# Performance work log

Hardware: AMD Instinct MI355X
Metric: run time of the kernel (lower is better)

## Reference

```python
import jax, jax.numpy as jnp
import numpy as np
import math

DROPOUT_P = 0.1

def setup_inputs() -> dict:
    key = jax.random.key(0)
    k1, k2, k3 = jax.random.split(key, 3)
    B, Lq, Lk, D = 8, 2048, 2048, 128
    x1 = jax.random.normal(k1, (B, Lq, D), dtype=jnp.float32)
    x2 = jax.random.normal(k2, (B, Lk, D), dtype=jnp.float32)
    qm = jnp.zeros((1, Lq, Lk), dtype=jnp.float32)  # additive attention mask
    u = jax.random.uniform(k3, (B, Lq, Lk), dtype=jnp.float32)  # dropout uniforms
    return {"x1": x1, "x2": x2, "qm": qm, "u": u}

def reference(x1, x2, qm, u):
    # scaled dot-product attention with additive mask + inverted dropout
    scale = 1.0 / math.sqrt(x1.shape[-1])
    qk = jnp.einsum('bqd,bkd->bqk', x1, x2) * scale + qm  # [B, Lq, Lk]
    attn = jax.nn.softmax(qk, axis=-1)
    keep = (u >= DROPOUT_P).astype(attn.dtype) / (1.0 - DROPOUT_P)
    attn = attn * keep
    out = jnp.einsum('bqk,bkd->bqd', attn, x2)  # [B, Lq, D]
    return out
```

## Files before the change

kernel.cpp:

```cpp
#include <hip/hip_runtime.h>
#include <hip/hip_bf16.h>
#include <stdint.h>

#define LQ 2048
#define LK 2048
#define DH 128
#define BQ 64
#define KB 128
#define NT (LK / KB)
#define KROW 136
#define LOG2E 1.44269504088896340736f
#define QSCALE 0.088388347648318447f

typedef __attribute__((ext_vector_type(8)))  short bf16x8;
typedef __attribute__((ext_vector_type(16))) float f32x16;
typedef __attribute__((ext_vector_type(4)))  float f32x4;

union FragAB { uint32_t u[4]; bf16x8 v; };

__device__ __forceinline__ uint32_t pack2_bf16(float lo, float hi) {
  union { __hip_bfloat16 b; uint16_t u; } a, c;
  a.b = __float2bfloat16(lo);
  c.b = __float2bfloat16(hi);
  return (uint32_t)a.u | ((uint32_t)c.u << 16);
}

__global__ __launch_bounds__(256)
void mask_kernel(const float* __restrict__ uu, uint32_t* __restrict__ maskp) {
  const int lane = threadIdx.x & 63;
  const int wid  = blockIdx.x * 4 + (threadIdx.x >> 6);
#pragma unroll 1
  for (int i = 0; i < 16; ++i) {
    const size_t F = ((size_t)i * 8192 + wid) * 256;
    float u0 = uu[F + 0 * 64 + lane];
    float u1 = uu[F + 1 * 64 + lane];
    float u2 = uu[F + 2 * 64 + lane];
    float u3 = uu[F + 3 * 64 + lane];
    uint64_t B0 = __ballot(u0 >= 0.1f);
    uint64_t B1 = __ballot(u1 >= 0.1f);
    uint64_t B2 = __ballot(u2 >= 0.1f);
    uint64_t B3 = __ballot(u3 >= 0.1f);
    if (lane < 8) {
      const int m = lane;
      uint64_t bb = (m < 2) ? B0 : (m < 4) ? B1 : (m < 6) ? B2 : B3;
      uint32_t val = (m & 1) ? (uint32_t)(bb >> 32) : (uint32_t)bb;
      const size_t row = F >> 11;
      const int c = (int)((F >> 5) & 63) + m;
      maskp[row * 64 + (size_t)((c & 3) * 16 + (c >> 2))] = val;
    }
  }
}

__global__ __launch_bounds__(256)
void qmt_kernel(const float* __restrict__ qm, uint16_t* __restrict__ qmt2) {
  const int kc = threadIdx.x & 63;
  const int q  = blockIdx.x * 4 + (threadIdx.x >> 6);
  f32x4 r[8];
  const float* src = qm + (size_t)q * 2048 + kc * 32;
#pragma unroll
  for (int c = 0; c < 8; ++c) r[c] = *(const f32x4*)(src + c * 4);
#pragma unroll
  for (int h = 0; h < 2; ++h) {
    uint32_t w[8];
#pragma unroll
    for (int i = 0; i < 8; ++i) {
      const int gi0 = 2 * i, gi1 = 2 * i + 1;
      const float v0 = r[h + (gi0 >> 2) * 2][gi0 & 3] * LOG2E;
      const float v1 = r[h + (gi1 >> 2) * 2][gi1 & 3] * LOG2E;
      w[i] = pack2_bf16(v0, v1);
    }
    uint16_t* dst = qmt2 + ((size_t)(kc * 2 + h) * 2048 + q) * 16;
    uint4 lo = {w[0], w[1], w[2], w[3]};
    uint4 hi = {w[4], w[5], w[6], w[7]};
    *(uint4*)dst = lo;
    *(uint4*)(dst + 8) = hi;
  }
}

__device__ __forceinline__ void stage_writes(uint16_t* Kb, uint16_t* Vb,
                                             const f32x4* st, int sbi, int sbj) {
#pragma unroll
  for (int j = 0; j < 2; ++j) {
    const int rowb = 4 * (sbi + 16 * j);
#pragma unroll
    for (int r = 0; r < 4; ++r) {
      f32x4 v = st[j * 4 + r];
      uint64_t pk = (uint64_t)pack2_bf16(v.x, v.y) |
                    ((uint64_t)pack2_bf16(v.z, v.w) << 32);
      *(uint64_t*)(Kb + (size_t)(rowb + r) * KROW + 4 * sbj) = pk;
    }
#pragma unroll
    for (int c = 0; c < 4; ++c) {
      uint64_t pv = (uint64_t)pack2_bf16(st[j * 4 + 0][c], st[j * 4 + 1][c]) |
                    ((uint64_t)pack2_bf16(st[j * 4 + 2][c], st[j * 4 + 3][c]) << 32);
      *(uint64_t*)(Vb + (size_t)(4 * sbj + c) * KROW + rowb) = pv;
    }
  }
}

__global__ __launch_bounds__(512, 2)
void fattn_kernel(const float* __restrict__ x1, const float* __restrict__ x2,
                  const uint32_t* __restrict__ maskp,
                  const uint16_t* __restrict__ qmt2,
                  float* __restrict__ out)
{
  __shared__ uint16_t ldsK[2][128 * KROW];
  __shared__ uint16_t ldsV[2][128 * KROW];

  const int tid  = threadIdx.x;
  const int wv   = tid >> 6;
  const int lane = tid & 63;
  const int ln   = lane & 31;
  const int h    = lane >> 5;
  const int qsub = wv & 1;
  const int ks   = wv >> 1;

  const int b    = blockIdx.x & 7;
  const int qblk = blockIdx.x >> 3;
  const int qrow = qblk * BQ + qsub * 32 + ln;

  FragAB qf[8];
  {
    const float* qp = x1 + ((size_t)(b * LQ + qrow)) * DH + h * 8;
    const float qs = QSCALE * LOG2E;
#pragma unroll
    for (int dc = 0; dc < 8; ++dc) {
      f32x4 a = *(const f32x4*)(qp + dc * 16);
      f32x4 c = *(const f32x4*)(qp + dc * 16 + 4);
      qf[dc].u[0] = pack2_bf16(a.x * qs, a.y * qs);
      qf[dc].u[1] = pack2_bf16(a.z * qs, a.w * qs);
      qf[dc].u[2] = pack2_bf16(c.x * qs, c.y * qs);
      qf[dc].u[3] = pack2_bf16(c.z * qs, c.w * qs);
    }
  }

  const int sbi = tid >> 5;
  const int sbj = tid & 31;
  const float* x2base = x2 + (size_t)b * LK * DH + sbj * 4;
  const uint32_t* maskrow = maskp + ((size_t)(b * LQ + qrow)) * 64 + ks * 16;

  f32x4 st[8];
#pragma unroll
  for (int j = 0; j < 2; ++j)
#pragma unroll
    for (int r = 0; r < 4; ++r)
      st[j * 4 + r] = *(const f32x4*)(x2base + (size_t)(4 * (sbi + 16 * j) + r) * DH);

  uint32_t mcur = maskrow[0];
  uint4 qc0, qc1;
  {
    const uint16_t* qp16 = qmt2 + (((size_t)(0 * 4 + ks) * 2 + h) * 2048 + qrow) * 16;
    qc0 = *(const uint4*)qp16;
    qc1 = *(const uint4*)(qp16 + 8);
  }

  stage_writes(ldsK[0], ldsV[0], st, sbi, sbj);
  __syncthreads();

  float m_run = -1e30f, l_run = 0.f;
  f32x16 acco[4];
#pragma unroll
  for (int d2 = 0; d2 < 4; ++d2)
#pragma unroll
    for (int i = 0; i < 16; ++i) acco[d2][i] = 0.f;

  for (int t = 0; t < NT; ++t) {
    const int cb = t & 1;
    const uint16_t* Kb = ldsK[cb];
    const uint16_t* Vb = ldsV[cb];
    const int kb = t * KB;

    uint32_t mnxt = 0; uint4 qn0, qn1;
    if (t + 1 < NT) {
#pragma unroll
      for (int j = 0; j < 2; ++j)
#pragma unroll
        for (int r = 0; r < 4; ++r)
          st[j * 4 + r] = *(const f32x4*)(x2base + (size_t)(kb + KB + 4 * (sbi + 16 * j) + r) * DH);
      mnxt = maskrow[t + 1];
      const uint16_t* qp16 = qmt2 + (((size_t)((t + 1) * 4 + ks) * 2 + h) * 2048 + qrow) * 16;
      qn0 = *(const uint4*)qp16;
      qn1 = *(const uint4*)(qp16 + 8);
    }

    f32x16 sacc;
#pragma unroll
    for (int i = 0; i < 16; ++i) sacc[i] = 0.f;
    const uint16_t* Krow = Kb + (size_t)(ks * 32 + ln) * KROW + h * 8;
#pragma unroll
    for (int dc = 0; dc < 8; ++dc) {
      bf16x8 af = *(const bf16x8*)(Krow + dc * 16);
      sacc = __builtin_amdgcn_mfma_f32_32x32x16_bf16(af, qf[dc].v, sacc, 0, 0, 0);
    }

#define ADDQM(W, I) { sacc[I] += __uint_as_float((W) << 16); \
                      sacc[I + 1] += __uint_as_float((W) & 0xffff0000u); }
    ADDQM(qc0.x, 0)  ADDQM(qc0.y, 2)  ADDQM(qc0.z, 4)  ADDQM(qc0.w, 6)
    ADDQM(qc1.x, 8)  ADDQM(qc1.y, 10) ADDQM(qc1.z, 12) ADDQM(qc1.w, 14)
#undef ADDQM

    float pm = sacc[0];
#pragma unroll
    for (int i = 1; i < 16; ++i) pm = fmaxf(pm, sacc[i]);
    pm = fmaxf(pm, __shfl_xor(pm, 32));
    const float mnew = fmaxf(m_run, pm);
    const float resc = __builtin_amdgcn_exp2f(m_run - mnew);
    m_run = mnew;
    float rs = 0.f;
#pragma unroll
    for (int i = 0; i < 16; ++i) {
      sacc[i] = __builtin_amdgcn_exp2f(sacc[i] - mnew);
      rs += sacc[i];
    }
    rs += __shfl_xor(rs, 32);
    l_run = l_run * resc + rs;

#pragma unroll
    for (int g = 0; g < 4; ++g)
#pragma unroll
      for (int j2 = 0; j2 < 4; ++j2) {
        const uint32_t keep = (mcur >> (h * 4 + g * 8 + j2)) & 1u;
        sacc[g * 4 + j2] = keep ? sacc[g * 4 + j2] : 0.f;
      }

    uint32_t pr[4][2], sw[4][2];
#pragma unroll
    for (int g = 0; g < 4; ++g) {
      pr[g][0] = pack2_bf16(sacc[4 * g + 0], sacc[4 * g + 1]);
      pr[g][1] = pack2_bf16(sacc[4 * g + 2], sacc[4 * g + 3]);
      sw[g][0] = __shfl_xor(pr[g][0], 32);
      sw[g][1] = __shfl_xor(pr[g][1], 32);
    }
    FragAB bfr[2];
#pragma unroll
    for (int c = 0; c < 2; ++c) {
      bfr[c].u[0] = h ? sw[2 * c + 1][0] : pr[2 * c][0];
      bfr[c].u[1] = h ? sw[2 * c + 1][1] : pr[2 * c][1];
      bfr[c].u[2] = h ? pr[2 * c + 1][0] : sw[2 * c][0];
      bfr[c].u[3] = h ? pr[2 * c + 1][1] : sw[2 * c][1];
    }

#pragma unroll
    for (int d2 = 0; d2 < 4; ++d2)
#pragma unroll
      for (int i = 0; i < 16; ++i) acco[d2][i] *= resc;

#pragma unroll
    for (int d2 = 0; d2 < 4; ++d2) {
      const uint16_t* Vrow = Vb + (size_t)(d2 * 32 + ln) * KROW + ks * 32 + h * 8;
#pragma unroll
      for (int c = 0; c < 2; ++c) {
        bf16x8 av = *(const bf16x8*)(Vrow + c * 16);
        acco[d2] = __builtin_amdgcn_mfma_f32_32x32x16_bf16(av, bfr[c].v, acco[d2], 0, 0, 0);
      }
    }

    if (t + 1 < NT) {
      stage_writes(ldsK[cb ^ 1], ldsV[cb ^ 1], st, sbi, sbj);
      mcur = mnxt; qc0 = qn0; qc1 = qn1;
    }
    __syncthreads();
  }

  float* scr = (wv < 4) ? ((float*)ldsK + (size_t)wv * 4224)
                        : ((float*)ldsV + (size_t)(wv - 4) * 4224);
  scr[lane]      = m_run;
  scr[64 + lane] = l_run;
#pragma unroll
  for (int d2 = 0; d2 < 4; ++d2)
#pragma unroll
    for (int g = 0; g < 4; ++g) {
      f32x4 vv;
#pragma unroll
      for (int j2 = 0; j2 < 4; ++j2) vv[j2] = acco[d2][g * 4 + j2];
      *(f32x4*)(scr + 128 + (size_t)(d2 * 4 + g) * 256 + lane * 4) = vv;
    }
  __syncthreads();

  if (wv < 2) {
    const float* rg[4];
#pragma unroll
    for (int s2 = 0; s2 < 4; ++s2) {
      const int r = qsub + 2 * s2;
      rg[s2] = (r < 4) ? ((const float*)ldsK + (size_t)r * 4224)
                       : ((const float*)ldsV + (size_t)(r - 4) * 4224);
    }
    const float ms0 = rg[0][lane], ms1 = rg[1][lane], ms2 = rg[2][lane], ms3 = rg[3][lane];
    const float ls0 = rg[0][64 + lane], ls1 = rg[1][64 + lane];
    const float ls2 = rg[2][64 + lane], ls3 = rg[3][64 + lane];
    const float mM = fmaxf(fmaxf(ms0, ms1), fmaxf(ms2, ms3));
    const float e0 = __builtin_amdgcn_exp2f(ms0 - mM);
    const float e1 = __builtin_amdgcn_exp2f(ms1 - mM);
    const float e2 = __builtin_amdgcn_exp2f(ms2 - mM);
    const float e3 = __builtin_amdgcn_exp2f(ms3 - mM);
    const float lM = e0 * ls0 + e1 * ls1 + e2 * ls2 + e3 * ls3;
    const float inv = (1.0f / 0.9f) / lM;
    float* op = out + ((size_t)(b * LQ + qrow)) * DH;
#pragma unroll
    for (int d2 = 0; d2 < 4; ++d2)
#pragma unroll
      for (int g = 0; g < 4; ++g) {
        const size_t off = 128 + (size_t)(d2 * 4 + g) * 256 + lane * 4;
        f32x4 a4 = e0 * *(const f32x4*)(rg[0] + off)
                 + e1 * *(const f32x4*)(rg[1] + off)
                 + e2 * *(const f32x4*)(rg[2] + off)
                 + e3 * *(const f32x4*)(rg[3] + off);
        a4 = a4 * inv;
        *(f32x4*)(op + d2 * 32 + 8 * g + 4 * h) = a4;
      }
  }
}

extern "C" void kernel_launch(void* const* d_in, const int* in_sizes, int n_in,
                              void* d_out, int out_size, void* d_ws, size_t ws_size,
                              hipStream_t stream) {
  (void)in_sizes; (void)n_in; (void)out_size; (void)ws_size;
  const float* x1 = (const float*)d_in[0];
  const float* x2 = (const float*)d_in[1];
  const float* qm = (const float*)d_in[2];
  const float* u  = (const float*)d_in[3];
  float* out = (float*)d_out;

  uint32_t* maskp = (uint32_t*)d_ws;
  uint16_t* qmt2  = (uint16_t*)((char*)d_ws + (4u << 20));

  mask_kernel<<<dim3(2048), dim3(256), 0, stream>>>(u, maskp);
  qmt_kernel<<<dim3(512), dim3(256), 0, stream>>>(qm, qmt2);
  fattn_kernel<<<dim3(256), dim3(512), 0, stream>>>(x1, x2, maskp, qmt2, out);
}
```

Before: 269.5 us.

## Fuse dropout mask generation into attention kernel and swizzle V LDS layout

Removes the separate mask_kernel pass: the attention kernel now streams the dropout uniforms directly with nontemporal loads, prefetched one tile ahead, and builds the keep bitmask in-register via wave ballots. This drops one kernel launch and avoids writing and re-reading a packed mask buffer. In exchange each thread holds 32 extra float registers for the current and next tile, which may raise register pressure. The change also XOR-swizzles V tile writes and reads in LDS to reduce bank conflicts, and raises wave priority around the MFMA sections with s_setprio.

```diff
diff --git a/kernel.cpp b/kernel.cpp
--- a/kernel.cpp
+++ b/kernel.cpp
@@ -26,32 +26,6 @@
 }
 
 __global__ __launch_bounds__(256)
-void mask_kernel(const float* __restrict__ uu, uint32_t* __restrict__ maskp) {
-  const int lane = threadIdx.x & 63;
-  const int wid  = blockIdx.x * 4 + (threadIdx.x >> 6);
-#pragma unroll 1
-  for (int i = 0; i < 16; ++i) {
-    const size_t F = ((size_t)i * 8192 + wid) * 256;
-    float u0 = uu[F + 0 * 64 + lane];
-    float u1 = uu[F + 1 * 64 + lane];
-    float u2 = uu[F + 2 * 64 + lane];
-    float u3 = uu[F + 3 * 64 + lane];
-    uint64_t B0 = __ballot(u0 >= 0.1f);
-    uint64_t B1 = __ballot(u1 >= 0.1f);
-    uint64_t B2 = __ballot(u2 >= 0.1f);
-    uint64_t B3 = __ballot(u3 >= 0.1f);
-    if (lane < 8) {
-      const int m = lane;
-      uint64_t bb = (m < 2) ? B0 : (m < 4) ? B1 : (m < 6) ? B2 : B3;
-      uint32_t val = (m & 1) ? (uint32_t)(bb >> 32) : (uint32_t)bb;
-      const size_t row = F >> 11;
-      const int c = (int)((F >> 5) & 63) + m;
-      maskp[row * 64 + (size_t)((c & 3) * 16 + (c >> 2))] = val;
-    }
-  }
-}
-
-__global__ __launch_bounds__(256)
 void qmt_kernel(const float* __restrict__ qm, uint16_t* __restrict__ qmt2) {
   const int kc = threadIdx.x & 63;
   const int q  = blockIdx.x * 4 + (threadIdx.x >> 6);
@@ -93,14 +67,15 @@
     for (int c = 0; c < 4; ++c) {
       uint64_t pv = (uint64_t)pack2_bf16(st[j * 4 + 0][c], st[j * 4 + 1][c]) |
                     ((uint64_t)pack2_bf16(st[j * 4 + 2][c], st[j * 4 + 3][c]) << 32);
-      *(uint64_t*)(Vb + (size_t)(4 * sbj + c) * KROW + rowb) = pv;
+      const size_t off = ((size_t)(4 * sbj + c) * KROW + rowb) ^ (size_t)((sbj & 7) << 3);
+      *(uint64_t*)(Vb + off) = pv;
     }
   }
 }
 
 __global__ __launch_bounds__(512, 2)
 void fattn_kernel(const float* __restrict__ x1, const float* __restrict__ x2,
-                  const uint32_t* __restrict__ maskp,
+                  const float* __restrict__ uu,
                   const uint16_t* __restrict__ qmt2,
                   float* __restrict__ out)
 {
@@ -117,7 +92,8 @@
 
   const int b    = blockIdx.x & 7;
   const int qblk = blockIdx.x >> 3;
-  const int qrow = qblk * BQ + qsub * 32 + ln;
+  const int qbase = qblk * BQ + qsub * 32;
+  const int qrow  = qbase + ln;
 
   FragAB qf[8];
   {
@@ -137,7 +113,8 @@
   const int sbi = tid >> 5;
   const int sbj = tid & 31;
   const float* x2base = x2 + (size_t)b * LK * DH + sbj * 4;
-  const uint32_t* maskrow = maskp + ((size_t)(b * LQ + qrow)) * 64 + ks * 16;
+  const float* ub = uu + ((size_t)(b * LQ + qbase + h)) * LK + ks * 32 + ln;
+  const int vxor = ((ln >> 2) & 7) << 3;
 
   f32x4 st[8];
 #pragma unroll
@@ -146,7 +123,11 @@
     for (int r = 0; r < 4; ++r)
       st[j * 4 + r] = *(const f32x4*)(x2base + (size_t)(4 * (sbi + 16 * j) + r) * DH);
 
-  uint32_t mcur = maskrow[0];
+  float ucur[16];
+#pragma unroll
+  for (int i = 0; i < 16; ++i)
+    ucur[i] = __builtin_nontemporal_load(ub + (size_t)(2 * i) * LK);
+
   uint4 qc0, qc1;
   {
     const uint16_t* qp16 = qmt2 + (((size_t)(0 * 4 + ks) * 2 + h) * 2048 + qrow) * 16;
@@ -170,14 +151,16 @@
     const uint16_t* Vb = ldsV[cb];
     const int kb = t * KB;
 
-    uint32_t mnxt = 0; uint4 qn0, qn1;
+    float unxt[16]; uint4 qn0, qn1;
     if (t + 1 < NT) {
 #pragma unroll
       for (int j = 0; j < 2; ++j)
 #pragma unroll
         for (int r = 0; r < 4; ++r)
           st[j * 4 + r] = *(const f32x4*)(x2base + (size_t)(kb + KB + 4 * (sbi + 16 * j) + r) * DH);
-      mnxt = maskrow[t + 1];
+#pragma unroll
+      for (int i = 0; i < 16; ++i)
+        unxt[i] = __builtin_nontemporal_load(ub + (size_t)(kb + KB) + (size_t)(2 * i) * LK);
       const uint16_t* qp16 = qmt2 + (((size_t)((t + 1) * 4 + ks) * 2 + h) * 2048 + qrow) * 16;
       qn0 = *(const uint4*)qp16;
       qn1 = *(const uint4*)(qp16 + 8);
@@ -187,11 +170,13 @@
 #pragma unroll
     for (int i = 0; i < 16; ++i) sacc[i] = 0.f;
     const uint16_t* Krow = Kb + (size_t)(ks * 32 + ln) * KROW + h * 8;
+    __builtin_amdgcn_s_setprio(1);
 #pragma unroll
     for (int dc = 0; dc < 8; ++dc) {
       bf16x8 af = *(const bf16x8*)(Krow + dc * 16);
       sacc = __builtin_amdgcn_mfma_f32_32x32x16_bf16(af, qf[dc].v, sacc, 0, 0, 0);
     }
+    __builtin_amdgcn_s_setprio(0);
 
 #define ADDQM(W, I) { sacc[I] += __uint_as_float((W) << 16); \
                       sacc[I + 1] += __uint_as_float((W) & 0xffff0000u); }
@@ -215,11 +200,18 @@
     rs += __shfl_xor(rs, 32);
     l_run = l_run * resc + rs;
 
+    uint32_t M = 0;
+#pragma unroll
+    for (int i = 0; i < 16; ++i) {
+      unsigned long long bi = __ballot(ucur[i] >= 0.1f);
+      uint32_t sel = (ln & 1) ? (uint32_t)(bi >> 32) : (uint32_t)bi;
+      M = ((ln >> 1) == i) ? sel : M;
+    }
 #pragma unroll
     for (int g = 0; g < 4; ++g)
 #pragma unroll
       for (int j2 = 0; j2 < 4; ++j2) {
-        const uint32_t keep = (mcur >> (h * 4 + g * 8 + j2)) & 1u;
+        const uint32_t keep = (M >> (h * 4 + g * 8 + j2)) & 1u;
         sacc[g * 4 + j2] = keep ? sacc[g * 4 + j2] : 0.f;
       }
 
@@ -245,19 +237,23 @@
 #pragma unroll
       for (int i = 0; i < 16; ++i) acco[d2][i] *= resc;
 
+    __builtin_amdgcn_s_setprio(1);
 #pragma unroll
     for (int d2 = 0; d2 < 4; ++d2) {
-      const uint16_t* Vrow = Vb + (size_t)(d2 * 32 + ln) * KROW + ks * 32 + h * 8;
 #pragma unroll
       for (int c = 0; c < 2; ++c) {
-        bf16x8 av = *(const bf16x8*)(Vrow + c * 16);
+        const size_t voff = (((size_t)(d2 * 32 + ln)) * KROW + ks * 32 + h * 8 + c * 16) ^ (size_t)vxor;
+        bf16x8 av = *(const bf16x8*)(Vb + voff);
         acco[d2] = __builtin_amdgcn_mfma_f32_32x32x16_bf16(av, bfr[c].v, acco[d2], 0, 0, 0);
       }
     }
+    __builtin_amdgcn_s_setprio(0);
 
     if (t + 1 < NT) {
       stage_writes(ldsK[cb ^ 1], ldsV[cb ^ 1], st, sbi, sbj);
-      mcur = mnxt; qc0 = qn0; qc1 = qn1;
+#pragma unroll
+      for (int i = 0; i < 16; ++i) ucur[i] = unxt[i];
+      qc0 = qn0; qc1 = qn1;
     }
     __syncthreads();
   }
@@ -295,7 +291,11 @@
     const float e3 = __builtin_amdgcn_exp2f(ms3 - mM);
     const float lM = e0 * ls0 + e1 * ls1 + e2 * ls2 + e3 * ls3;
     const float inv = (1.0f / 0.9f) / lM;
-    float* op = out + ((size_t)(b * LQ + qrow)) * DH;
+    float* op = out + ((size_t)(b * LQ + qblk * BQ + qsub * 32 + lane % 32)) * DH;
+    (void)op;
+    const int lq = lane & 31;
+    float* op2 = out + ((size_t)(b * LQ + qblk * BQ + qsub * 32 + lq)) * DH;
+    const int hh = lane >> 5;
 #pragma unroll
     for (int d2 = 0; d2 < 4; ++d2)
 #pragma unroll
@@ -306,7 +306,7 @@
                  + e2 * *(const f32x4*)(rg[2] + off)
                  + e3 * *(const f32x4*)(rg[3] + off);
         a4 = a4 * inv;
-        *(f32x4*)(op + d2 * 32 + 8 * g + 4 * h) = a4;
+        *(f32x4*)(op2 + d2 * 32 + 8 * g + 4 * hh) = a4;
       }
   }
 }
@@ -321,10 +321,8 @@
   const float* u  = (const float*)d_in[3];
   float* out = (float*)d_out;
 
-  uint32_t* maskp = (uint32_t*)d_ws;
-  uint16_t* qmt2  = (uint16_t*)((char*)d_ws + (4u << 20));
-
-  mask_kernel<<<dim3(2048), dim3(256), 0, stream>>>(u, maskp);
+  uint16_t* qmt2 = (uint16_t*)d_ws;
+
   qmt_kernel<<<dim3(512), dim3(256), 0, stream>>>(qm, qmt2);
-  fattn_kernel<<<dim3(256), dim3(512), 0, stream>>>(x1, x2, maskp, qmt2, out);
-}
+  fattn_kernel<<<dim3(256), dim3(512), 0, stream>>>(x1, x2, u, qmt2, out);
+}
```

Measured after the change: 245.1 us. 1.1x faster.
